# Optimization experiments

Measured on AMD Instinct MI355X. Metric: run time of the kernel, lower is better.

Reference implementation:

```python
import jax, jax.numpy as jnp
import numpy as np

HEADS = 16
DIM_HEAD = 64
MASK_VALUE = -(np.finfo(np.float32).max / 2)


def setup_inputs() -> dict:
    key = jax.random.key(0)
    k1, k2, k3 = jax.random.split(key, 3)
    B, N, D = 2, 2048, 1024
    inner = HEADS * DIM_HEAD
    x = jax.random.normal(k1, (B, N, D), dtype=jnp.float32)
    w_qkv = jax.random.normal(k2, (D, 3 * inner), dtype=jnp.float32) * (D ** -0.5)
    w_out = jax.random.normal(k3, (inner, D), dtype=jnp.float32) * (inner ** -0.5)
    b_out = jnp.zeros((D,), dtype=jnp.float32)
    return {"x": x, "w_qkv": w_qkv, "w_out": w_out, "b_out": b_out}


def reference(x, w_qkv, w_out, b_out):
    B, N, D = x.shape
    H, Dh = HEADS, DIM_HEAD
    qkv = x @ w_qkv                                   # [B, N, 3*H*Dh]
    q, k, v = jnp.split(qkv, 3, axis=-1)
    # [B, N, H*Dh] -> [B, H, N, Dh]
    split_heads = lambda t: t.reshape(B, N, H, Dh).transpose(0, 2, 1, 3)
    q, k, v = split_heads(q), split_heads(k), split_heads(v)
    scale = Dh ** -0.5
    sim = jnp.einsum('bhid,bhjd->bhij', q, k) * scale  # [B, H, N, N]
    # causal additive mask: MASK_VALUE above the diagonal
    causal = jnp.triu(jnp.ones((N, N), dtype=bool), k=1)
    mask = jnp.where(causal, jnp.float32(MASK_VALUE), 0.0)
    sim = sim + mask[None, None, :, :]
    attn = jax.nn.softmax(sim, axis=-1)
    out = jnp.einsum('bhij,bhjd->bhid', attn, v)       # [B, H, N, Dh]
    out = out.transpose(0, 2, 1, 3).reshape(B, N, H * Dh)
    return out @ w_out + b_out
```

## Files before the change

### kernel.cpp

```cpp
#include <hip/hip_runtime.h>
#include <hip/hip_bf16.h>

typedef __attribute__((ext_vector_type(4)))  float    f32x4;
typedef __attribute__((ext_vector_type(16))) float    f32x16;
typedef __attribute__((ext_vector_type(8)))  short    bf16x8;
typedef __attribute__((ext_vector_type(4)))  short    s16x4;
typedef __attribute__((ext_vector_type(4)))  unsigned u32x4;

#define B_    2
#define N_    2048
#define D_    1024
#define HEADS 16
#define DH    64
#define M_    4096
#define INNER 1024

static __device__ __forceinline__ short f2bf(float f) {
    __hip_bfloat16 h = __float2bfloat16(f);
    return __builtin_bit_cast(short, h);
}
static __device__ __forceinline__ float bf2f(short s) {
    unsigned u = ((unsigned)(unsigned short)s) << 16;
    return __builtin_bit_cast(float, u);
}
static __device__ __forceinline__ unsigned pack2(float lo, float hi) {
    return ((unsigned)(unsigned short)f2bf(lo)) |
           (((unsigned)(unsigned short)f2bf(hi)) << 16);
}
static __device__ __forceinline__ unsigned cvtpk(float lo, float hi) {
    unsigned r;
    asm("v_cvt_pk_bf16_f32 %0, %1, %2" : "=v"(r) : "v"(lo), "v"(hi));
    return r;
}
static __device__ __forceinline__ void plswap(unsigned& a, unsigned& b) {
    asm("v_permlane32_swap_b32 %0, %1" : "+v"(a), "+v"(b));
}
static __device__ __forceinline__ float fexp2(float x) {
    float r;
    asm("v_exp_f32 %0, %1" : "=v"(r) : "v"(x));
    return r;
}
static __device__ __forceinline__ float flog2(float x) {
    float r;
    asm("v_log_f32 %0, %1" : "=v"(r) : "v"(x));
    return r;
}
static __device__ __forceinline__ float vmax16(f32x16 v) {
    float a = fmaxf(fmaxf(v[0], v[1]), fmaxf(v[2], v[3]));
    float b = fmaxf(fmaxf(v[4], v[5]), fmaxf(v[6], v[7]));
    float c = fmaxf(fmaxf(v[8], v[9]), fmaxf(v[10], v[11]));
    float d = fmaxf(fmaxf(v[12], v[13]), fmaxf(v[14], v[15]));
    return fmaxf(fmaxf(a, b), fmaxf(c, d));
}
static __device__ __forceinline__ float vsum16(f32x16 v) {
    float a = (v[0] + v[1]) + (v[2] + v[3]);
    float b = (v[4] + v[5]) + (v[6] + v[7]);
    float c = (v[8] + v[9]) + (v[10] + v[11]);
    float d = (v[12] + v[13]) + (v[14] + v[15]);
    return (a + b) + (c + d);
}

static __device__ __forceinline__ void transpose_tile(const float* __restrict__ in,
                                                      short* __restrict__ out,
                                                      int R, int C, int bx32, int by32,
                                                      float* t ) {
    int tx = threadIdx.x & 31, ty = threadIdx.x >> 5;
    int bx = bx32 * 32, by = by32 * 32;
#pragma unroll
    for (int j = 0; j < 32; j += 8)
        t[(ty + j) * 33 + tx] = in[(long)(by + ty + j) * C + bx + tx];
    __syncthreads();
#pragma unroll
    for (int j = 0; j < 32; j += 8)
        out[(long)(bx + ty + j) * R + by + tx] = f2bf(t[tx * 33 + ty + j]);
}

__global__ void __launch_bounds__(256) prep_k(const float* __restrict__ x,
                                              short* __restrict__ xb,
                                              const float* __restrict__ w_qkv,
                                              short* __restrict__ wqkvT,
                                              const float* __restrict__ w_out,
                                              short* __restrict__ woutT) {
    __shared__ float t[32 * 33];
    int bid = blockIdx.x;
    if (bid < 4096) {
        int i = bid * 256 + threadIdx.x;
        f32x4 v = ((const f32x4*)x)[i];
        s16x4 o;
        o[0] = f2bf(v[0]); o[1] = f2bf(v[1]); o[2] = f2bf(v[2]); o[3] = f2bf(v[3]);
        ((s16x4*)xb)[i] = o;
    } else if (bid < 4096 + 3072) {
        int tt = bid - 4096;
        transpose_tile(w_qkv, wqkvT, 1024, 3072, tt % 96, tt / 96, t);
    } else {
        int tt = bid - 7168;
        transpose_tile(w_out, woutT, 1024, 1024, tt % 32, tt / 32, t);
    }
}

template <int ROWS>
static __device__ __forceinline__ void stage_swz(const short* __restrict__ src,
                                                 int ldElems, short* lds, int tid) {
    constexpr int CH = (ROWS * 128) / (256 * 16);
#pragma unroll
    for (int c = 0; c < CH; ++c) {
        int o   = (tid + c * 256) * 16;
        int row = o >> 7;
        int kb  = (o & 127) ^ ((row & 7) << 4);
        const char* g = (const char*)src + (long)row * ldElems * 2 + kb;
        __builtin_amdgcn_global_load_lds(
            (const __attribute__((address_space(1))) void*)g,
            (__attribute__((address_space(3))) void*)((char*)lds + o), 16, 0, 0);
    }
}
static __device__ __forceinline__ bf16x8 lds_frag(const short* lds, int row, int kbyte) {
    return *(const bf16x8*)((const char*)lds + (row << 7) + (kbyte ^ ((row & 7) << 4)));
}

__global__ void __launch_bounds__(256) gemm_k(const short* __restrict__ A,
                                              const short* __restrict__ Bt, int K,
                                              short* __restrict__ q_out,
                                              short* __restrict__ k_out,
                                              short* __restrict__ v_out) {
    __shared__ __align__(16) short As[128 * 64];
    __shared__ __align__(16) short Bs[128 * 64];
    int tid = threadIdx.x;
    int lane = tid & 63, w = tid >> 6, wr = w >> 1, wc = w & 1;
    int l15 = lane & 15, lg = lane >> 4;
    int nx = gridDim.x;
    int flat = blockIdx.y * nx + blockIdx.x;
    int total = nx * gridDim.y;
    int cpx = total >> 3;
    int swz = (flat & 7) * cpx + (flat >> 3);
    int row0 = (swz / nx) * 128, col0 = (swz % nx) * 128;

    f32x4 acc[4][4] = {};

    for (int k0 = 0; k0 < K; k0 += 64) {
        stage_swz<128>(A + (long)row0 * K + k0, K, As, tid);
        stage_swz<128>(Bt + (long)col0 * K + k0, K, Bs, tid);
        __syncthreads();
#pragma unroll
        for (int kb = 0; kb < 2; ++kb) {
            int kbyte = kb * 64 + (lg << 4);
            bf16x8 af[4], bfr[4];
#pragma unroll
            for (int mr = 0; mr < 4; ++mr)
                af[mr] = lds_frag(As, wr * 64 + mr * 16 + l15, kbyte);
#pragma unroll
            for (int nr = 0; nr < 4; ++nr)
                bfr[nr] = lds_frag(Bs, wc * 64 + nr * 16 + l15, kbyte);
#pragma unroll
            for (int mr = 0; mr < 4; ++mr)
#pragma unroll
                for (int nr = 0; nr < 4; ++nr)
                    acc[mr][nr] = __builtin_amdgcn_mfma_f32_16x16x32_bf16(
                        af[mr], bfr[nr], acc[mr][nr], 0, 0, 0);
        }
        __syncthreads();
    }

#pragma unroll
    for (int mr = 0; mr < 4; ++mr)
#pragma unroll
        for (int nr = 0; nr < 4; ++nr) {
            int gr0 = row0 + wr * 64 + mr * 16 + (lg << 2);
            int gc  = col0 + wc * 64 + nr * 16 + l15;
            int which = gc >> 10, rem = gc & 1023;
            int h = rem >> 6, d = rem & 63;
            int b = gr0 >> 11, nn0 = gr0 & 2047;
            long bh32 = (long)(b * HEADS + h) * 32;
            if (which == 2) {
                int t = nn0 >> 6, ks = (nn0 >> 4) & 3, hb = (nn0 >> 3) & 1;
                long off = (((bh32 + t) * 2 + (d >> 5)) * 4 + ks) * 512
                           + ((hb << 5) + (d & 31)) * 8 + (nn0 & 4);
                s16x4 pk;
#pragma unroll
                for (int reg = 0; reg < 4; ++reg) pk[reg] = f2bf(acc[mr][nr][reg]);
                *(s16x4*)(v_out + off) = pk;
            } else if (which == 1) {
                int dk = d >> 4, hb = (d >> 3) & 1, j = d & 7;
                int t = nn0 >> 6, ss = (nn0 >> 5) & 1;
                long fbase = ((bh32 + t) * 2 + ss) * 4 + dk;
#pragma unroll
                for (int reg = 0; reg < 4; ++reg) {
                    int l31k = (nn0 + reg) & 31;
                    k_out[fbase * 512 + ((hb << 5) + l31k) * 8 + j] =
                        f2bf(acc[mr][nr][reg]);
                }
            } else {
                float sc = 0.180336880f;
#pragma unroll
                for (int reg = 0; reg < 4; ++reg) {
                    int gr = gr0 + reg;
                    int bb = gr >> 11, nn = gr & 2047;
                    q_out[((long)(bb * HEADS + h) * N_ + nn) * DH + d] =
                        f2bf(acc[mr][nr][reg] * sc);
                }
            }
        }
}

__global__ void __launch_bounds__(256) gemm2_k(const short* __restrict__ A,
                                               const short* __restrict__ Bt,
                                               float* __restrict__ f_out,
                                               const float* __restrict__ bias) {
    __shared__ __align__(16) short As[128 * 64];
    __shared__ __align__(16) short Bs[64 * 64];
    int tid = threadIdx.x;
    int lane = tid & 63, w = tid >> 6, wr = w >> 1, wc = w & 1;
    int l15 = lane & 15, lg = lane >> 4;
    const int K = 1024;
    int flat = blockIdx.y * 16 + blockIdx.x;
    int swz = (flat & 7) * 64 + (flat >> 3);
    int row0 = (swz >> 4) * 128, col0 = (swz & 15) * 64;

    f32x4 acc[4][2] = {};

    for (int k0 = 0; k0 < K; k0 += 64) {
        stage_swz<128>(A + (long)row0 * K + k0, K, As, tid);
        stage_swz<64>(Bt + (long)col0 * K + k0, K, Bs, tid);
        __syncthreads();
#pragma unroll
        for (int kb = 0; kb < 2; ++kb) {
            int kbyte = kb * 64 + (lg << 4);
            bf16x8 af[4], bfr[2];
#pragma unroll
            for (int mr = 0; mr < 4; ++mr)
                af[mr] = lds_frag(As, wr * 64 + mr * 16 + l15, kbyte);
#pragma unroll
            for (int nc = 0; nc < 2; ++nc)
                bfr[nc] = lds_frag(Bs, wc * 32 + nc * 16 + l15, kbyte);
#pragma unroll
            for (int mr = 0; mr < 4; ++mr)
#pragma unroll
                for (int nc = 0; nc < 2; ++nc)
                    acc[mr][nc] = __builtin_amdgcn_mfma_f32_16x16x32_bf16(
                        af[mr], bfr[nc], acc[mr][nc], 0, 0, 0);
        }
        __syncthreads();
    }

#pragma unroll
    for (int mr = 0; mr < 4; ++mr)
#pragma unroll
        for (int nc = 0; nc < 2; ++nc) {
            int gc = col0 + wc * 32 + nc * 16 + l15;
            float bv = bias[gc];
#pragma unroll
            for (int reg = 0; reg < 4; ++reg) {
                int gr = row0 + wr * 64 + mr * 16 + (lg << 2) + reg;
                f_out[(long)gr * D_ + gc] = acc[mr][nc][reg] + bv;
            }
        }
}

__global__ void __launch_bounds__(256, 3) attn_k(const short* __restrict__ Qb,
                                                 const short* __restrict__ Kf,
                                                 const short* __restrict__ Vf,
                                                 short* __restrict__ O0,
                                                 short* __restrict__ O1,
                                                 float* __restrict__ lse) {
    __shared__ __align__(16) short Ep[4][2048];
    int tid = threadIdx.x, lane = tid & 63, w = tid >> 6;
    int l31 = lane & 31, hbit = lane >> 5;
    int bq = blockIdx.x;
    int q4 = bq >> 8, rest = bq & 255;
    int bh = rest >> 3, p = rest & 7;
    int x = (q4 < 2) ? (15 - p) : p;
    int seg = q4 & 1;
    int t0 = seg ? (x + 1) : 0;
    int t1 = seg ? (2 * x + 2) : (x + 1);

    const short* Qh = Qb + (long)bh * N_ * DH;
    const short* Kh = Kf + (long)bh * 32 * 4096;
    const short* Vh = Vf + (long)bh * 32 * 4096;
    int lofs = lane * 8;

    int q0 = x * 128 + w * 32;
    int qg = q0 + l31;
    int t1w = min(t1, ((q0 + 31) >> 6) + 1);

    bf16x8 qf[4];
#pragma unroll
    for (int kf = 0; kf < 4; ++kf)
        qf[kf] = *(const bf16x8*)(Qh + (long)qg * DH + kf * 16 + hbit * 8);

    f32x16 o[2] = {};
    float m = -1e30f, l = 0.f;

    for (int t = t0; t < t1w; ++t) {
        const short* kb = Kh + (long)t * 4096;
        const short* vb = Vh + (long)t * 4096;
        int khb = t * 64;

        bf16x8 kfr[2][4];
#pragma unroll
        for (int ss = 0; ss < 2; ++ss)
#pragma unroll
            for (int dk = 0; dk < 4; ++dk)
                kfr[ss][dk] = *(const bf16x8*)(kb + (ss * 4 + dk) * 512 + lofs);

        f32x16 S[2] = {};
        __builtin_amdgcn_s_setprio(1);
#pragma unroll
        for (int ss = 0; ss < 2; ++ss)
#pragma unroll
            for (int dk = 0; dk < 4; ++dk)
                S[ss] = __builtin_amdgcn_mfma_f32_32x32x16_bf16(
                    kfr[ss][dk], qf[dk], S[ss], 0, 0, 0);
        __builtin_amdgcn_s_setprio(0);

        bf16x8 vf[2][4];
#pragma unroll
        for (int df = 0; df < 2; ++df)
#pragma unroll
            for (int ks = 0; ks < 4; ++ks)
                vf[df][ks] = *(const bf16x8*)(vb + (df * 4 + ks) * 512 + lofs);

        if (khb + 63 > q0) {
            int kvl = khb + 4 * hbit;
#pragma unroll
            for (int ss = 0; ss < 2; ++ss)
#pragma unroll
                for (int r = 0; r < 16; ++r) {
                    int kv = kvl + 32 * ss + (r & 3) + 8 * (r >> 2);
                    if (kv > qg) S[ss][r] = -1e30f;
                }
        }

        float pm = fmaxf(vmax16(S[0]), vmax16(S[1]));
        pm = fmaxf(pm, __shfl_xor(pm, 32));
        if (!__all(pm <= m + 8.0f)) {
            float mn = fmaxf(m, pm);
            float corr = fexp2(m - mn);
            m = mn;
            l *= corr;
#pragma unroll
            for (int df = 0; df < 2; ++df)
#pragma unroll
                for (int r = 0; r < 16; ++r) o[df][r] *= corr;
        }
#pragma unroll
        for (int ss = 0; ss < 2; ++ss)
#pragma unroll
            for (int r = 0; r < 16; ++r)
                S[ss][r] = fexp2(S[ss][r] - m);
        l += vsum16(S[0]) + vsum16(S[1]);

        __builtin_amdgcn_s_setprio(1);
#pragma unroll
        for (int ss = 0; ss < 2; ++ss) {
#pragma unroll
            for (int hs = 0; hs < 2; ++hs) {
                unsigned w0 = cvtpk(S[ss][hs * 8 + 0], S[ss][hs * 8 + 1]);
                unsigned w1 = cvtpk(S[ss][hs * 8 + 2], S[ss][hs * 8 + 3]);
                unsigned w2 = cvtpk(S[ss][hs * 8 + 4], S[ss][hs * 8 + 5]);
                unsigned w3 = cvtpk(S[ss][hs * 8 + 6], S[ss][hs * 8 + 7]);
                plswap(w0, w2);
                plswap(w1, w3);
                bf16x8 pfrag = __builtin_bit_cast(bf16x8, (u32x4){w0, w1, w2, w3});
                int ks = ss * 2 + hs;
#pragma unroll
                for (int df = 0; df < 2; ++df)
                    o[df] = __builtin_amdgcn_mfma_f32_32x32x16_bf16(
                        vf[df][ks], pfrag, o[df], 0, 0, 0);
            }
        }
        __builtin_amdgcn_s_setprio(0);
    }

    l += __shfl_xor(l, 32);
    float linv = (l > 0.f) ? 1.0f / l : 0.f;
    if (hbit == 0)
        lse[seg * (32 * N_) + bh * N_ + qg] =
            (l > 0.f) ? (m + flog2(l)) : -__builtin_inff();

    char* Epw = (char*)&Ep[w][0];
#pragma unroll
    for (int df = 0; df < 2; ++df)
#pragma unroll
        for (int r = 0; r < 16; r += 2) {
            unsigned pk = pack2(o[df][r] * linv, o[df][r + 1] * linv);
            int d = df * 32 + (r & 3) + 8 * (r >> 2) + 4 * hbit;
            int cb = d * 2;
            *(unsigned*)(Epw + (l31 << 7) + (cb ^ ((l31 & 7) << 4))) = pk;
        }
    __syncthreads();

    int b = bh >> 4, h = bh & 15;
    int lr = lane >> 1, lc = lane & 1;
    const char* rbase = Epw + (lr << 7);
    long orow = seg ? ((long)(bh * N_ + q0 + lr)) * 64 + lc * 32
                    : ((long)(b * N_ + q0 + lr)) * INNER + h * DH + lc * 32;
    short* dst = seg ? O1 : O0;
#pragma unroll
    for (int j = 0; j < 4; ++j) {
        int cb = lc * 64 + j * 16;
        bf16x8 vv = *(const bf16x8*)(rbase + (cb ^ ((lr & 7) << 4)));
        *(bf16x8*)(dst + orow + j * 8) = vv;
    }
}

__global__ void __launch_bounds__(256) merge_k(short* __restrict__ Ab,
                                               const short* __restrict__ O1,
                                               const float* __restrict__ lse) {
    int gid = blockIdx.x * 256 + threadIdx.x;
    int row = gid >> 3, d0 = (gid & 7) * 8;
    int bh = row >> 11, n = row & 2047;
    float l0 = lse[row];
    float l1 = lse[32 * N_ + row];
    float Mx = fmaxf(l0, l1);
    float w0 = fexp2(l0 - Mx), w1 = fexp2(l1 - Mx);
    float inv = 1.0f / (w0 + w1);
    w0 *= inv; w1 *= inv;
    int b = bh >> 4, h = bh & 15;
    long a_off = ((long)(b * N_ + n) * HEADS + h) * DH + d0;
    long o_off = (long)row * DH + d0;
    bf16x8 v0 = *(const bf16x8*)(Ab + a_off);
    bf16x8 v1 = *(const bf16x8*)(O1 + o_off);
    bf16x8 r;
#pragma unroll
    for (int i = 0; i < 8; ++i)
        r[i] = f2bf(w0 * bf2f(v0[i]) + w1 * bf2f(v1[i]));
    *(bf16x8*)(Ab + a_off) = r;
}


extern "C" void kernel_launch(void* const* d_in, const int* in_sizes, int n_in,
                              void* d_out, int out_size, void* d_ws, size_t ws_size,
                              hipStream_t stream) {
    const float* x     = (const float*)d_in[0];
    const float* w_qkv = (const float*)d_in[1];
    const float* w_out = (const float*)d_in[2];
    const float* b_out = (const float*)d_in[3];
    float* out = (float*)d_out;

    char* ws = (char*)d_ws;
    const size_t MB = 1024 * 1024;
    short* xb    = (short*)(ws + 0 * MB);
    short* wqkvT = (short*)(ws + 8 * MB);
    short* woutT = (short*)(ws + 14 * MB);
    short* Qb    = (short*)(ws + 16 * MB);
    short* Kfb   = (short*)(ws + 24 * MB);
    short* Vfb   = (short*)(ws + 32 * MB);
    short* Ab    = (short*)(ws + 40 * MB);
    short* O1    = (short*)(ws + 0 * MB);
    float* lse   = (float*)(ws + 8 * MB);

    prep_k<<<dim3(4096 + 3072 + 1024), 256, 0, stream>>>(
        x, xb, w_qkv, wqkvT, w_out, woutT);

    gemm_k<<<dim3(3072 / 128, M_ / 128), 256, 0, stream>>>(
        xb, wqkvT, 1024, Qb, Kfb, Vfb);

    attn_k<<<dim3(1024), 256, 0, stream>>>(Qb, Kfb, Vfb, Ab, O1, lse);
    merge_k<<<dim3((32 * N_ * 8) / 256), 256, 0, stream>>>(Ab, O1, lse);

    gemm2_k<<<dim3(1024 / 64, M_ / 128), 256, 0, stream>>>(Ab, woutT, out, b_out);
}
```

Baseline: 101.6 us.

## Rewrite QKV GEMM as 256x256 tile, 8-wave, double-buffered pipelined kernel

The QKV projection GEMM moves from 128x128 tiles with 4 waves and a synchronous load-then-compute loop to 256x256 tiles with 8 waves. LDS is double-buffered and loaded in half-tile pieces that are interleaved across four compute phases. Each phase uses explicit vmcnt waits, barriers and setprio so global-to-LDS loads overlap MFMA work. The goal is more reuse per loaded byte and hidden load latency, at the cost of a much smaller grid (192 blocks), heavier register and LDS use per block, and fragile hand-tuned synchronisation.

```diff
diff --git a/kernel.cpp b/kernel.cpp
--- a/kernel.cpp
+++ b/kernel.cpp
@@ -113,92 +113,150 @@
             (__attribute__((address_space(3))) void*)((char*)lds + o), 16, 0, 0);
     }
 }
+static __device__ __forceinline__ void stage_half(const short* __restrict__ src,
+                                                  int ldElems, short* lds, int tid) {
+#pragma unroll
+    for (int c = 0; c < 2; ++c) {
+        int o   = (tid + c * 512) * 16;
+        int row = o >> 7;
+        int kb  = (o & 127) ^ ((row & 7) << 4);
+        const char* g = (const char*)src + (long)row * ldElems * 2 + kb;
+        __builtin_amdgcn_global_load_lds(
+            (const __attribute__((address_space(1))) void*)g,
+            (__attribute__((address_space(3))) void*)((char*)lds + o), 16, 0, 0);
+    }
+}
 static __device__ __forceinline__ bf16x8 lds_frag(const short* lds, int row, int kbyte) {
     return *(const bf16x8*)((const char*)lds + (row << 7) + (kbyte ^ ((row & 7) << 4)));
 }
 
-__global__ void __launch_bounds__(256) gemm_k(const short* __restrict__ A,
-                                              const short* __restrict__ Bt, int K,
-                                              short* __restrict__ q_out,
-                                              short* __restrict__ k_out,
-                                              short* __restrict__ v_out) {
-    __shared__ __align__(16) short As[128 * 64];
-    __shared__ __align__(16) short Bs[128 * 64];
+#define G1_PHASE(qa, qb, STAGE)                                                  \
+    {                                                                            \
+        bf16x8 af[2][4], bfr[2][2];                                              \
+        _Pragma("unroll") for (int kb = 0; kb < 2; ++kb) {                       \
+            int kbyte = kb * 64 + (lg << 4);                                     \
+            _Pragma("unroll") for (int mp = 0; mp < 4; ++mp)                     \
+                af[kb][mp] = lds_frag(Asb, (qa) * 128 + wm * 64 + mp * 16 + l15, \
+                                      kbyte);                                    \
+            _Pragma("unroll") for (int np = 0; np < 2; ++np)                     \
+                bfr[kb][np] = lds_frag(Bsb, (qb) * 128 + wn * 32 + np * 16 + l15,\
+                                       kbyte);                                   \
+        }                                                                        \
+        STAGE;                                                                   \
+        __builtin_amdgcn_s_barrier();                                            \
+        asm volatile("s_waitcnt lgkmcnt(0)" ::: "memory");                       \
+        __builtin_amdgcn_sched_barrier(0);                                       \
+        __builtin_amdgcn_s_setprio(1);                                           \
+        _Pragma("unroll") for (int kb = 0; kb < 2; ++kb)                         \
+            _Pragma("unroll") for (int mp = 0; mp < 4; ++mp)                     \
+                _Pragma("unroll") for (int np = 0; np < 2; ++np)                 \
+                    acc[qa][mp][qb][np] =                                        \
+                        __builtin_amdgcn_mfma_f32_16x16x32_bf16(                 \
+                            af[kb][mp], bfr[kb][np], acc[qa][mp][qb][np],        \
+                            0, 0, 0);                                            \
+        __builtin_amdgcn_s_setprio(0);                                           \
+        __builtin_amdgcn_s_barrier();                                            \
+    }
+
+__global__ void __launch_bounds__(512, 2) gemm_k(const short* __restrict__ A,
+                                                 const short* __restrict__ Bt, int K,
+                                                 short* __restrict__ q_out,
+                                                 short* __restrict__ k_out,
+                                                 short* __restrict__ v_out) {
+    __shared__ __align__(16) short As[2 * 256 * 64];
+    __shared__ __align__(16) short Bs[2 * 256 * 64];
     int tid = threadIdx.x;
-    int lane = tid & 63, w = tid >> 6, wr = w >> 1, wc = w & 1;
+    int lane = tid & 63, w = tid >> 6;
+    int wm = w >> 2, wn = w & 3;
     int l15 = lane & 15, lg = lane >> 4;
     int nx = gridDim.x;
     int flat = blockIdx.y * nx + blockIdx.x;
     int total = nx * gridDim.y;
     int cpx = total >> 3;
     int swz = (flat & 7) * cpx + (flat >> 3);
-    int row0 = (swz / nx) * 128, col0 = (swz % nx) * 128;
-
-    f32x4 acc[4][4] = {};
-
-    for (int k0 = 0; k0 < K; k0 += 64) {
-        stage_swz<128>(A + (long)row0 * K + k0, K, As, tid);
-        stage_swz<128>(Bt + (long)col0 * K + k0, K, Bs, tid);
-        __syncthreads();
-#pragma unroll
-        for (int kb = 0; kb < 2; ++kb) {
-            int kbyte = kb * 64 + (lg << 4);
-            bf16x8 af[4], bfr[4];
-#pragma unroll
-            for (int mr = 0; mr < 4; ++mr)
-                af[mr] = lds_frag(As, wr * 64 + mr * 16 + l15, kbyte);
-#pragma unroll
-            for (int nr = 0; nr < 4; ++nr)
-                bfr[nr] = lds_frag(Bs, wc * 64 + nr * 16 + l15, kbyte);
-#pragma unroll
-            for (int mr = 0; mr < 4; ++mr)
-#pragma unroll
-                for (int nr = 0; nr < 4; ++nr)
-                    acc[mr][nr] = __builtin_amdgcn_mfma_f32_16x16x32_bf16(
-                        af[mr], bfr[nr], acc[mr][nr], 0, 0, 0);
-        }
-        __syncthreads();
-    }
-
-#pragma unroll
-    for (int mr = 0; mr < 4; ++mr)
-#pragma unroll
-        for (int nr = 0; nr < 4; ++nr) {
-            int gr0 = row0 + wr * 64 + mr * 16 + (lg << 2);
-            int gc  = col0 + wc * 64 + nr * 16 + l15;
-            int which = gc >> 10, rem = gc & 1023;
-            int h = rem >> 6, d = rem & 63;
-            int b = gr0 >> 11, nn0 = gr0 & 2047;
-            long bh32 = (long)(b * HEADS + h) * 32;
-            if (which == 2) {
-                int t = nn0 >> 6, ks = (nn0 >> 4) & 3, hb = (nn0 >> 3) & 1;
-                long off = (((bh32 + t) * 2 + (d >> 5)) * 4 + ks) * 512
-                           + ((hb << 5) + (d & 31)) * 8 + (nn0 & 4);
-                s16x4 pk;
-#pragma unroll
-                for (int reg = 0; reg < 4; ++reg) pk[reg] = f2bf(acc[mr][nr][reg]);
-                *(s16x4*)(v_out + off) = pk;
-            } else if (which == 1) {
-                int dk = d >> 4, hb = (d >> 3) & 1, j = d & 7;
-                int t = nn0 >> 6, ss = (nn0 >> 5) & 1;
-                long fbase = ((bh32 + t) * 2 + ss) * 4 + dk;
-#pragma unroll
-                for (int reg = 0; reg < 4; ++reg) {
-                    int l31k = (nn0 + reg) & 31;
-                    k_out[fbase * 512 + ((hb << 5) + l31k) * 8 + j] =
-                        f2bf(acc[mr][nr][reg]);
-                }
-            } else {
-                float sc = 0.180336880f;
-#pragma unroll
-                for (int reg = 0; reg < 4; ++reg) {
-                    int gr = gr0 + reg;
-                    int bb = gr >> 11, nn = gr & 2047;
-                    q_out[((long)(bb * HEADS + h) * N_ + nn) * DH + d] =
-                        f2bf(acc[mr][nr][reg] * sc);
-                }
+    int row0 = (swz / nx) * 256, col0 = (swz % nx) * 256;
+
+    const int NT = K >> 6;
+    const short* A0r = A + (long)row0 * K;
+    const short* A1r = A + (long)(row0 + 128) * K;
+    const short* B0r = Bt + (long)col0 * K;
+    const short* B1r = Bt + (long)(col0 + 128) * K;
+
+    f32x4 acc[2][4][2][2] = {};
+
+    stage_half(A0r,      K, As,         tid);
+    stage_half(B0r,      K, Bs,         tid);
+    stage_half(A1r,      K, As + 8192,  tid);
+    stage_half(B1r,      K, Bs + 8192,  tid);
+    stage_half(A0r + 64, K, As + 16384, tid);
+    stage_half(B0r + 64, K, Bs + 16384, tid);
+    asm volatile("s_waitcnt vmcnt(4)" ::: "memory");
+    __builtin_amdgcn_s_barrier();
+    __builtin_amdgcn_sched_barrier(0);
+
+    for (int T = 0; T < NT; ++T) {
+        int buf = T & 1;
+        short* Asb = As + buf * 16384;
+        short* Bsb = Bs + buf * 16384;
+        short* Asn = As + (buf ^ 1) * 16384;
+        short* Bsn = Bs + (buf ^ 1) * 16384;
+        int k1 = (T + 1) * 64, k2 = (T + 2) * 64;
+        bool s1 = (T + 1) < NT, s2 = (T + 2) < NT;
+
+        G1_PHASE(0, 0, if (s1) stage_half(A1r + k1, K, Asn + 8192, tid));
+        G1_PHASE(0, 1, if (s1) stage_half(B1r + k1, K, Bsn + 8192, tid));
+        G1_PHASE(1, 0, if (s2) stage_half(A0r + k2, K, Asb, tid));
+        G1_PHASE(1, 1, if (s2) stage_half(B0r + k2, K, Bsb, tid));
+
+        if (s2) asm volatile("s_waitcnt vmcnt(4)" ::: "memory");
+        else    asm volatile("s_waitcnt vmcnt(0)" ::: "memory");
+        __builtin_amdgcn_s_barrier();
+        __builtin_amdgcn_sched_barrier(0);
+    }
+
+#pragma unroll
+    for (int qa = 0; qa < 2; ++qa)
+#pragma unroll
+    for (int mp = 0; mp < 4; ++mp)
+#pragma unroll
+    for (int qb = 0; qb < 2; ++qb)
+#pragma unroll
+    for (int np = 0; np < 2; ++np) {
+        int gr0 = row0 + qa * 128 + wm * 64 + mp * 16 + (lg << 2);
+        int gc  = col0 + qb * 128 + wn * 32 + np * 16 + l15;
+        f32x4 av = acc[qa][mp][qb][np];
+        int which = gc >> 10, rem = gc & 1023;
+        int h = rem >> 6, d = rem & 63;
+        int b = gr0 >> 11, nn0 = gr0 & 2047;
+        long bh32 = (long)(b * HEADS + h) * 32;
+        if (which == 2) {
+            int t = nn0 >> 6, ks = (nn0 >> 4) & 3, hb = (nn0 >> 3) & 1;
+            long off = (((bh32 + t) * 2 + (d >> 5)) * 4 + ks) * 512
+                       + ((hb << 5) + (d & 31)) * 8 + (nn0 & 4);
+            s16x4 pk;
+#pragma unroll
+            for (int reg = 0; reg < 4; ++reg) pk[reg] = f2bf(av[reg]);
+            *(s16x4*)(v_out + off) = pk;
+        } else if (which == 1) {
+            int dk = d >> 4, hb = (d >> 3) & 1, j = d & 7;
+            int t = nn0 >> 6, ss = (nn0 >> 5) & 1;
+            long fbase = ((bh32 + t) * 2 + ss) * 4 + dk;
+#pragma unroll
+            for (int reg = 0; reg < 4; ++reg) {
+                int l31k = (nn0 + reg) & 31;
+                k_out[fbase * 512 + ((hb << 5) + l31k) * 8 + j] = f2bf(av[reg]);
             }
-        }
+        } else {
+            float sc = 0.180336880f;
+#pragma unroll
+            for (int reg = 0; reg < 4; ++reg) {
+                int gr = gr0 + reg;
+                int bb = gr >> 11, nn = gr & 2047;
+                q_out[((long)(bb * HEADS + h) * N_ + nn) * DH + d] =
+                    f2bf(av[reg] * sc);
+            }
+        }
+    }
 }
 
 __global__ void __launch_bounds__(256) gemm2_k(const short* __restrict__ A,
@@ -451,7 +509,7 @@
     prep_k<<<dim3(4096 + 3072 + 1024), 256, 0, stream>>>(
         x, xb, w_qkv, wqkvT, w_out, woutT);
 
-    gemm_k<<<dim3(3072 / 128, M_ / 128), 256, 0, stream>>>(
+    gemm_k<<<dim3(3072 / 256, M_ / 256), 512, 0, stream>>>(
         xb, wqkvT, 1024, Qb, Kfb, Vfb);
 
     attn_k<<<dim3(1024), 256, 0, stream>>>(Qb, Kfb, Vfb, Ab, O1, lse);
```

Result: slower. 108.6 us (+6.9%).

## Split attention KV range into four segments and merge four partials

Applied to the files above, without the earlier changes.

Each query tile's key range is now split into four segments instead of two, so the attention kernel launches twice as many blocks. The goal is better occupancy and load balance across CUs in the causal flash-decoding split. In exchange there is more partial-output traffic to two extra workspace buffers, and the merge kernel does more work combining four partials with LSE weights. Segments for small query tiles may be empty (l=0 gives lse=-inf), and these are handled by the existing -inf path.

```diff
diff --git a/kernel.cpp b/kernel.cpp
--- a/kernel.cpp
+++ b/kernel.cpp
@@ -260,17 +260,21 @@
                                                  const short* __restrict__ Vf,
                                                  short* __restrict__ O0,
                                                  short* __restrict__ O1,
+                                                 short* __restrict__ O2,
+                                                 short* __restrict__ O3,
                                                  float* __restrict__ lse) {
     __shared__ __align__(16) short Ep[4][2048];
     int tid = threadIdx.x, lane = tid & 63, w = tid >> 6;
     int l31 = lane & 31, hbit = lane >> 5;
     int bq = blockIdx.x;
-    int q4 = bq >> 8, rest = bq & 255;
+    int hi = bq >> 8;
+    int rest = bq & 255;
     int bh = rest >> 3, p = rest & 7;
-    int x = (q4 < 2) ? (15 - p) : p;
-    int seg = q4 & 1;
-    int t0 = seg ? (x + 1) : 0;
-    int t1 = seg ? (2 * x + 2) : (x + 1);
+    int x = (hi < 4) ? (15 - p) : p;
+    int seg = hi & 3;
+    int L = 2 * x + 2;
+    int t0 = (seg * L) >> 2;
+    int t1 = ((seg + 1) * L) >> 2;
 
     const short* Qh = Qb + (long)bh * N_ * DH;
     const short* Kh = Kf + (long)bh * 32 * 4096;
@@ -391,9 +395,15 @@
     int b = bh >> 4, h = bh & 15;
     int lr = lane >> 1, lc = lane & 1;
     const char* rbase = Epw + (lr << 7);
-    long orow = seg ? ((long)(bh * N_ + q0 + lr)) * 64 + lc * 32
-                    : ((long)(b * N_ + q0 + lr)) * INNER + h * DH + lc * 32;
-    short* dst = seg ? O1 : O0;
+    short* dst;
+    long orow;
+    if (seg == 0) {
+        dst = O0;
+        orow = ((long)(b * N_ + q0 + lr)) * INNER + h * DH + lc * 32;
+    } else {
+        dst = (seg == 1) ? O1 : (seg == 2) ? O2 : O3;
+        orow = ((long)(bh * N_ + q0 + lr)) * 64 + lc * 32;
+    }
 #pragma unroll
     for (int j = 0; j < 4; ++j) {
         int cb = lc * 64 + j * 16;
@@ -404,25 +414,34 @@
 
 __global__ void __launch_bounds__(256) merge_k(short* __restrict__ Ab,
                                                const short* __restrict__ O1,
+                                               const short* __restrict__ O2,
+                                               const short* __restrict__ O3,
                                                const float* __restrict__ lse) {
+    const int SZ = 32 * N_;
     int gid = blockIdx.x * 256 + threadIdx.x;
     int row = gid >> 3, d0 = (gid & 7) * 8;
     int bh = row >> 11, n = row & 2047;
     float l0 = lse[row];
-    float l1 = lse[32 * N_ + row];
-    float Mx = fmaxf(l0, l1);
+    float l1 = lse[SZ + row];
+    float l2 = lse[2 * SZ + row];
+    float l3 = lse[3 * SZ + row];
+    float Mx = fmaxf(fmaxf(l0, l1), fmaxf(l2, l3));
     float w0 = fexp2(l0 - Mx), w1 = fexp2(l1 - Mx);
-    float inv = 1.0f / (w0 + w1);
-    w0 *= inv; w1 *= inv;
+    float w2 = fexp2(l2 - Mx), w3 = fexp2(l3 - Mx);
+    float inv = 1.0f / (w0 + w1 + w2 + w3);
+    w0 *= inv; w1 *= inv; w2 *= inv; w3 *= inv;
     int b = bh >> 4, h = bh & 15;
     long a_off = ((long)(b * N_ + n) * HEADS + h) * DH + d0;
     long o_off = (long)row * DH + d0;
     bf16x8 v0 = *(const bf16x8*)(Ab + a_off);
     bf16x8 v1 = *(const bf16x8*)(O1 + o_off);
+    bf16x8 v2 = *(const bf16x8*)(O2 + o_off);
+    bf16x8 v3 = *(const bf16x8*)(O3 + o_off);
     bf16x8 r;
 #pragma unroll
     for (int i = 0; i < 8; ++i)
-        r[i] = f2bf(w0 * bf2f(v0[i]) + w1 * bf2f(v1[i]));
+        r[i] = f2bf(w0 * bf2f(v0[i]) + w1 * bf2f(v1[i]) +
+                    w2 * bf2f(v2[i]) + w3 * bf2f(v3[i]));
     *(bf16x8*)(Ab + a_off) = r;
 }
 
@@ -446,6 +465,8 @@
     short* Vfb   = (short*)(ws + 32 * MB);
     short* Ab    = (short*)(ws + 40 * MB);
     short* O1    = (short*)(ws + 0 * MB);
+    short* O2    = (short*)(ws + 48 * MB);
+    short* O3    = (short*)(ws + 56 * MB);
     float* lse   = (float*)(ws + 8 * MB);
 
     prep_k<<<dim3(4096 + 3072 + 1024), 256, 0, stream>>>(
@@ -454,8 +475,8 @@
     gemm_k<<<dim3(3072 / 128, M_ / 128), 256, 0, stream>>>(
         xb, wqkvT, 1024, Qb, Kfb, Vfb);
 
-    attn_k<<<dim3(1024), 256, 0, stream>>>(Qb, Kfb, Vfb, Ab, O1, lse);
-    merge_k<<<dim3((32 * N_ * 8) / 256), 256, 0, stream>>>(Ab, O1, lse);
+    attn_k<<<dim3(2048), 256, 0, stream>>>(Qb, Kfb, Vfb, Ab, O1, O2, O3, lse);
+    merge_k<<<dim3((32 * N_ * 8) / 256), 256, 0, stream>>>(Ab, O1, O2, O3, lse);
 
     gemm2_k<<<dim3(1024 / 64, M_ / 128), 256, 0, stream>>>(Ab, woutT, out, b_out);
 }
```

Measured after the change: 108.8 us. 1.07x slower.
